# Optimization experiments

Measured on AMD Instinct MI355X. Metric: run time of the kernel, lower is better.

Reference implementation:

```python
import jax, jax.numpy as jnp
import numpy as np

N_NODES = 100000
N_EDGES = 1600000
IN_DIM, HID_DIM, N_CLS = 500, 64, 16


def spline_conv(x, edge_index, edge_attr, w, root, bias):
    """SplineConv with dim=1, kernel_size=2, degree=1, aggr='add'.

    For K=2, m=1 open B-spline: v = pseudo * (K - m) = pseudo in [0,1],
    basis = [(1 - v), v] with kernel indices [0, 1].
    """
    v = jnp.clip(edge_attr[:, 0], 0.0, 1.0 - 1e-6)  # [E]
    src, dst = edge_index[0], edge_index[1]
    # Precompute per-node transforms for both kernel indices (dense GEMMs),
    # then gather per-edge instead of gathering [in,out] weight matrices.
    xw0 = x @ w[0]  # [N, out]
    xw1 = x @ w[1]  # [N, out]
    msg = (1.0 - v)[:, None] * xw0[src] + v[:, None] * xw1[src]  # [E, out]
    agg = jax.ops.segment_sum(msg, dst, num_segments=x.shape[0])  # [N, out]
    return agg + x @ root + bias


def setup_inputs() -> dict:
    key = jax.random.key(0)
    ks = jax.random.split(key, 8)
    x = jax.random.normal(ks[0], (N_NODES, IN_DIM), dtype=jnp.float32)
    edge_index = jax.random.randint(ks[1], (2, N_EDGES), 0, N_NODES, dtype=jnp.int32)
    edge_attr = jax.random.uniform(ks[2], (N_EDGES, 1), dtype=jnp.float32)
    s1 = 1.0 / np.sqrt(IN_DIM)
    s2 = 1.0 / np.sqrt(HID_DIM)
    w1 = jax.random.normal(ks[3], (2, IN_DIM, HID_DIM), dtype=jnp.float32) * s1
    root1 = jax.random.normal(ks[4], (IN_DIM, HID_DIM), dtype=jnp.float32) * s1
    b1 = jnp.zeros((HID_DIM,), dtype=jnp.float32)
    w2 = jax.random.normal(ks[5], (2, HID_DIM, N_CLS), dtype=jnp.float32) * s2
    root2 = jax.random.normal(ks[6], (HID_DIM, N_CLS), dtype=jnp.float32) * s2
    b2 = jnp.zeros((N_CLS,), dtype=jnp.float32)
    return {"x": x, "edge_index": edge_index, "edge_attr": edge_attr,
            "w1": w1, "root1": root1, "b1": b1,
            "w2": w2, "root2": root2, "b2": b2}


def reference(x, edge_index, edge_attr, w1, root1, b1, w2, root2, b2):
    # dropout is identity at inference time
    h = spline_conv(x, edge_index, edge_attr, w1, root1, b1)
    h = jax.nn.relu(h)
    h = spline_conv(h, edge_index, edge_attr, w2, root2, b2)
    return jax.nn.log_softmax(h, axis=1)
```

## Files before the change

### kernel.cpp

```cpp
#include <hip/hip_runtime.h>
#include <math.h>

#define N_NODES 100000
#define N_EDGES 1600000
#define IN_DIM 500
#define HID 64
#define NCLS 16
#define KP 512
#define NSTEPS 16
#define NBUK 391
#define NPAD (NBUK * 256)
#define EPB_B 4096
#define NBB ((N_EDGES + EPB_B - 1) / EPB_B)
#define CAP 8192

typedef __attribute__((ext_vector_type(8))) short short8;
typedef __attribute__((ext_vector_type(4))) float f32x4;

__device__ __forceinline__ unsigned short f2bf(float f) {
    unsigned u = __builtin_bit_cast(unsigned, f);
    return (unsigned short)((u + 0x7FFFu + ((u >> 16) & 1u)) >> 16);
}
__device__ __forceinline__ float bf2f(unsigned short s) {
    unsigned u = ((unsigned)s) << 16;
    return __builtin_bit_cast(float, u);
}
__device__ __forceinline__ unsigned pack2(unsigned short a, unsigned short b) {
    return (unsigned)a | ((unsigned)b << 16);
}
__device__ __forceinline__ void gload16(const void* g, void* l) {
    __builtin_amdgcn_global_load_lds(
        (const __attribute__((address_space(1))) unsigned*)g,
        (__attribute__((address_space(3))) unsigned*)l, 16, 0, 0);
}

__global__ __launch_bounds__(256) void k0_bt(
    const float* __restrict__ w1, const float* __restrict__ root1,
    unsigned short* __restrict__ Bt, int* __restrict__ bkcur)
{
    const int b = blockIdx.x;
    if (b == 192) {
        for (int i = threadIdx.x; i < NBUK; i += 256) bkcur[i] = i * CAP;
        return;
    }
    const float* src;
    int c;
    if (b < 64)        { src = w1;                c = b; }
    else if (b < 128)  { src = w1 + IN_DIM * HID; c = b - 64; }
    else               { src = root1;             c = b - 128; }
    for (int k = threadIdx.x; k < KP; k += 256) {
        float v = (k < IN_DIM) ? src[k * HID + c] : 0.f;
        Bt[b * KP + k] = f2bf(v);
    }
}

union K1Smem {
    struct { float A[4][64 * 32]; unsigned short B[4][192 * 32]; } s;
    unsigned short O[64 * 264];
    struct { int hcnt[NBUK]; int hbase[NBUK]; } bk;
};

__global__ __launch_bounds__(256) void fat_bucket_k1(
    const int* __restrict__ ei, const float* __restrict__ ea,
    int* __restrict__ bkcur, uint2* __restrict__ epk,
    const float* __restrict__ x, const unsigned short* __restrict__ Bt,
    unsigned short* __restrict__ xw01, float* __restrict__ aggH)
{
    __shared__ K1Smem sm;
    const int tid = threadIdx.x;
    const int bi = blockIdx.x;

    if (bi % 5 == 0) {
        const int start = (bi / 5) * EPB_B;
        const int eend = min(start + EPB_B, N_EDGES);

        for (int i = tid; i < NBUK; i += 256) sm.bk.hcnt[i] = 0;
        __syncthreads();

#pragma unroll
        for (int j = 0; j < EPB_B / 256; ++j) {
            const int e = start + j * 256 + tid;
            if (e < eend) atomicAdd(&sm.bk.hcnt[ei[N_EDGES + e] >> 8], 1);
        }
        __syncthreads();

        for (int b = tid; b < NBUK; b += 256) {
            const int c = sm.bk.hcnt[b];
            sm.bk.hbase[b] = c ? atomicAdd(&bkcur[b], c) : 0;
        }
        __syncthreads();
        for (int i = tid; i < NBUK; i += 256) sm.bk.hcnt[i] = 0;
        __syncthreads();

#pragma unroll
        for (int j = 0; j < EPB_B / 256; ++j) {
            const int e = start + j * 256 + tid;
            if (e < eend) {
                const int src = ei[e];
                const int dst = ei[N_EDGES + e];
                const float v = fminf(fmaxf(ea[e], 0.f), 1.f - 1e-6f);
                const unsigned vq = (unsigned)(v * 16777216.0f);
                const int bk = dst >> 8;
                const int r = atomicAdd(&sm.bk.hcnt[bk], 1);
                epk[sm.bk.hbase[bk] + r] =
                    make_uint2((unsigned)src, ((unsigned)(dst & 255) << 24) | vq);
            }
        }
        return;
    }

    const int row0 = (bi - (bi + 4) / 5) * 64;
    const int w = tid >> 6;
    const int l = tid & 63;
    const int l16 = l & 15;
    const int koct = l >> 4;
    const int wr = w >> 1;
    const int wc = w & 1;

    f32x4 acc[2][6];
#pragma unroll
    for (int i = 0; i < 2; ++i)
#pragma unroll
        for (int j = 0; j < 6; ++j) acc[i][j] = (f32x4){0.f, 0.f, 0.f, 0.f};

    const int aChunk4 = (l & 7) * 4;
    const float* aBase[2];
    int aLdsOff[2];
#pragma unroll
    for (int i = 0; i < 2; ++i) {
        const int rowl = (2 * w + i) * 8 + (l >> 3);
        int grow = row0 + rowl;
        if (grow > N_NODES - 1) grow = N_NODES - 1;
        aBase[i] = x + (size_t)grow * IN_DIM;
        aLdsOff[i] = (2 * w + i) * 256;
    }
    const unsigned short* bBase[3];
    int bLdsOff[3];
#pragma unroll
    for (int i = 0; i < 3; ++i) {
        const int coll = (3 * w + i) * 16 + (l >> 2);
        bBase[i] = Bt + (size_t)coll * KP + (l & 3) * 8;
        bLdsOff[i] = (3 * w + i) * 512;
    }

    auto ISSUE = [&](int s) {
        const int k0 = s * 32;
        const int buf = s & 3;
#pragma unroll
        for (int i = 0; i < 2; ++i) {
            int gk = k0 + aChunk4; if (gk > IN_DIM - 4) gk = IN_DIM - 4;
            gload16(aBase[i] + gk, &sm.s.A[buf][aLdsOff[i]]);
        }
#pragma unroll
        for (int i = 0; i < 3; ++i)
            gload16(bBase[i] + k0, &sm.s.B[buf][bLdsOff[i]]);
    };

    ISSUE(0);
    ISSUE(1);
    ISSUE(2);

#pragma unroll
    for (int s = 0; s < NSTEPS; ++s) {
        if (s < NSTEPS - 2)       asm volatile("s_waitcnt vmcnt(10)" ::: "memory");
        else if (s == NSTEPS - 2) asm volatile("s_waitcnt vmcnt(5)" ::: "memory");
        else                      asm volatile("s_waitcnt vmcnt(0)" ::: "memory");
        __builtin_amdgcn_s_barrier();
        asm volatile("" ::: "memory");
        if (s + 3 < NSTEPS) ISSUE(s + 3);

        const int buf = s & 3;
        const float* LA = sm.s.A[buf];
        const unsigned short* LB = sm.s.B[buf];
        short8 af[2];
#pragma unroll
        for (int rb = 0; rb < 2; ++rb) {
            const int r = wr * 32 + rb * 16 + l16;
            f32x4 f0 = *(const f32x4*)&LA[r * 32 + koct * 8];
            f32x4 f1 = *(const f32x4*)&LA[r * 32 + koct * 8 + 4];
            short8 a;
            a[0] = (short)f2bf(f0[0]); a[1] = (short)f2bf(f0[1]);
            a[2] = (short)f2bf(f0[2]); a[3] = (short)f2bf(f0[3]);
            a[4] = (short)f2bf(f1[0]); a[5] = (short)f2bf(f1[1]);
            a[6] = (short)f2bf(f1[2]); a[7] = (short)f2bf(f1[3]);
            af[rb] = a;
        }
#pragma unroll
        for (int cf = 0; cf < 6; ++cf) {
            const int c = wc * 96 + cf * 16 + l16;
            short8 bfg = *(const short8*)&LB[c * 32 + koct * 8];
            acc[0][cf] = __builtin_amdgcn_mfma_f32_16x16x32_bf16(af[0], bfg, acc[0][cf], 0, 0, 0);
            acc[1][cf] = __builtin_amdgcn_mfma_f32_16x16x32_bf16(af[1], bfg, acc[1][cf], 0, 0, 0);
        }
    }
    __syncthreads();

#pragma unroll
    for (int rb = 0; rb < 2; ++rb)
#pragma unroll
        for (int cf = 0; cf < 6; ++cf) {
            const int cg = wc * 96 + cf * 16 + l16;
            if (96 * wc + cf * 16 < 128) {
#pragma unroll
                for (int reg = 0; reg < 4; ++reg) {
                    const int rloc = wr * 32 + rb * 16 + koct * 4 + reg;
                    const int idx = (cg < 64) ? (2 * cg) : (2 * cg - 127);
                    sm.O[rloc * 264 + idx] = f2bf(acc[rb][cf][reg]);
                }
            } else {
#pragma unroll
                for (int reg = 0; reg < 4; ++reg) {
                    const int r = row0 + wr * 32 + rb * 16 + koct * 4 + reg;
                    if (r < N_NODES) aggH[(size_t)r * HID + (cg - 128)] = acc[rb][cf][reg];
                }
            }
        }
    __syncthreads();
    {
        const int row = tid >> 2, q = tid & 3;
        const int rg = row0 + row;
        if (rg < N_NODES) {
#pragma unroll
            for (int j = 0; j < 4; ++j) {
                uint4 v = *(const uint4*)&sm.O[row * 264 + q * 32 + j * 8];
                *(uint4*)&xw01[(size_t)rg * 128 + q * 32 + j * 8] = v;
            }
        }
    }
}

__global__ __launch_bounds__(256) void csr_place(
    const int* __restrict__ bkcur, const uint2* __restrict__ epk,
    uint2* __restrict__ epkS, int* __restrict__ off, int* __restrict__ deg)
{
    __shared__ uint2 buf[CAP];
    __shared__ int hist[256];
    __shared__ int sc[256];
    __shared__ int cur[256];

    const int b = blockIdx.x;
    const int tid = threadIdx.x;
    const int start = b * CAP;
    const int cnt = bkcur[b] - start;

    hist[tid] = 0;
    __syncthreads();
    for (int i = tid; i < cnt; i += 256)
        atomicAdd(&hist[epk[start + i].y >> 24], 1);
    __syncthreads();

    const int val = hist[tid];
    sc[tid] = val;
    for (int d = 1; d < 256; d <<= 1) {
        __syncthreads();
        int add = (tid >= d) ? sc[tid - d] : 0;
        __syncthreads();
        sc[tid] += add;
    }
    __syncthreads();
    const int myloc = sc[tid] - val;
    off[(b << 8) + tid] = start + myloc;
    deg[(b << 8) + tid] = val;
    cur[tid] = myloc;
    __syncthreads();

    for (int i = tid; i < cnt; i += 256) {
        const uint2 u = epk[start + i];
        const int dl = u.y >> 24;
        const float v = (float)(u.y & 0xFFFFFFu) * 5.9604644775390625e-8f;
        const int pos = atomicAdd(&cur[dl], 1);
        buf[pos] = make_uint2(u.x, __builtin_bit_cast(unsigned, v));
    }
    __syncthreads();

    for (int i = tid; i < cnt; i += 256)
        epkS[start + i] = buf[i];
}

__global__ __launch_bounds__(256) void agg1(
    const int* __restrict__ off, const int* __restrict__ deg,
    const uint2* __restrict__ epk, const unsigned* __restrict__ xw01_u,
    float* __restrict__ aggH)
{
    const int n = blockIdx.x * 4 + (threadIdx.x >> 6);
    if (n >= N_NODES) return;
    const int d = threadIdx.x & 63;
    const int start = off[n];
    const int dg = deg[n];

    float acc = aggH[(size_t)n * HID + d];
    for (int i = 0; i < dg; i += 8) {
        unsigned srcs[8];
        float w0[8], w1[8];
#pragma unroll
        for (int j = 0; j < 8; ++j) {
            const bool ok = (i + j) < dg;
            const int idx = ok ? (start + i + j) : start;
            const uint2 t = epk[idx];
            const float v = __builtin_bit_cast(float, t.y);
            srcs[j] = t.x;
            w0[j] = ok ? (1.f - v) : 0.f;
            w1[j] = ok ? v : 0.f;
        }
        unsigned g[8];
#pragma unroll
        for (int j = 0; j < 8; ++j) g[j] = xw01_u[(size_t)srcs[j] * 64 + d];
#pragma unroll
        for (int j = 0; j < 8; ++j) {
            acc += w0[j] * bf2f((unsigned short)(g[j] & 0xFFFF));
            acc += w1[j] * bf2f((unsigned short)(g[j] >> 16));
        }
    }
    aggH[(size_t)n * HID + d] = acc;
}

__global__ __launch_bounds__(256) void k3_relu_gemm(
    const float* __restrict__ aggH, const float* __restrict__ b1,
    const float* __restrict__ w2, const float* __restrict__ root2,
    unsigned* __restrict__ hw01_u, float* __restrict__ agg2)
{
    __shared__ float Ws[3 * HID * NCLS];
    __shared__ float Hs[16][HID];

    const int tid = threadIdx.x;
    for (int i = tid; i < 2 * HID * NCLS; i += 256) Ws[i] = w2[i];
    for (int i = tid; i < HID * NCLS; i += 256) Ws[2 * HID * NCLS + i] = root2[i];

    const int n0 = blockIdx.x * 16;
    for (int i = tid; i < 16 * HID; i += 256) {
        const int nl = i >> 6, k = i & 63;
        const float h = aggH[(size_t)(n0 + nl) * HID + k] + b1[k];
        Hs[nl][k] = fmaxf(h, 0.f);
    }
    __syncthreads();

    const int nl = tid >> 4;
    const int c = tid & 15;
    float a0 = 0.f, a1 = 0.f, a2 = 0.f;
#pragma unroll
    for (int k = 0; k < HID; ++k) {
        const float h = Hs[nl][k];
        a0 += h * Ws[0 * HID * NCLS + k * NCLS + c];
        a1 += h * Ws[1 * HID * NCLS + k * NCLS + c];
        a2 += h * Ws[2 * HID * NCLS + k * NCLS + c];
    }
    const size_t o = (size_t)(n0 + nl) * NCLS + c;
    hw01_u[o] = pack2(f2bf(a0), f2bf(a1));
    agg2[o] = a2;
}

__global__ __launch_bounds__(256) void agg2_sm(
    const int* __restrict__ off, const int* __restrict__ deg,
    const uint2* __restrict__ epk, const unsigned* __restrict__ hw01_u,
    const float* __restrict__ agg2, const float* __restrict__ b2,
    float* __restrict__ out)
{
    const int n = blockIdx.x * 16 + (threadIdx.x >> 4);
    const int c = threadIdx.x & 15;
    const int start = off[n];
    const int dg = deg[n];

    float acc = agg2[(size_t)n * NCLS + c];
    for (int i = 0; i < dg; i += 8) {
        unsigned srcs[8];
        float w0[8], w1[8];
#pragma unroll
        for (int j = 0; j < 8; ++j) {
            const bool ok = (i + j) < dg;
            const int idx = ok ? (start + i + j) : start;
            const uint2 t = epk[idx];
            const float v = __builtin_bit_cast(float, t.y);
            srcs[j] = t.x;
            w0[j] = ok ? (1.f - v) : 0.f;
            w1[j] = ok ? v : 0.f;
        }
        unsigned g[8];
#pragma unroll
        for (int j = 0; j < 8; ++j) g[j] = hw01_u[(size_t)srcs[j] * NCLS + c];
#pragma unroll
        for (int j = 0; j < 8; ++j) {
            acc += w0[j] * bf2f((unsigned short)(g[j] & 0xFFFF));
            acc += w1[j] * bf2f((unsigned short)(g[j] >> 16));
        }
    }

    const float z = acc + b2[c];
    float m = z;
#pragma unroll
    for (int s = 1; s < 16; s <<= 1) m = fmaxf(m, __shfl_xor(m, s, 64));
    const float e = expf(z - m);
    float ssum = e;
#pragma unroll
    for (int s = 1; s < 16; s <<= 1) ssum += __shfl_xor(ssum, s, 64);
    out[(size_t)n * NCLS + c] = (z - m) - logf(ssum);
}

extern "C" void kernel_launch(void* const* d_in, const int* in_sizes, int n_in,
                              void* d_out, int out_size, void* d_ws, size_t ws_size,
                              hipStream_t stream) {
    const float* x = (const float*)d_in[0];
    const int* ei = (const int*)d_in[1];
    const float* ea = (const float*)d_in[2];
    const float* w1 = (const float*)d_in[3];
    const float* root1 = (const float*)d_in[4];
    const float* b1 = (const float*)d_in[5];
    const float* w2 = (const float*)d_in[6];
    const float* root2 = (const float*)d_in[7];
    const float* b2 = (const float*)d_in[8];
    float* out = (float*)d_out;

    char* ws = (char*)d_ws;
    unsigned short* xw01 = (unsigned short*)ws;
    float* aggH = (float*)(ws + 25600000);
    unsigned* hw01_u = (unsigned*)(ws + 51200000);
    float* agg2 = (float*)(ws + 57600000);
    unsigned short* Bt = (unsigned short*)(ws + 64000000);
    int* off = (int*)(ws + 64300000);
    int* deg = (int*)(ws + 64800000);
    int* bkcur = (int*)(ws + 65300000);
    uint2* epk = (uint2*)(ws + 65400000);
    uint2* epkS = (uint2*)(ws + 91100000);

    k0_bt<<<193, 256, 0, stream>>>(w1, root1, Bt, bkcur);

    fat_bucket_k1<<<NBB + (N_NODES + 63) / 64, 256, 0, stream>>>(
        ei, ea, bkcur, epk, x, Bt, xw01, aggH);

    csr_place<<<NBUK, 256, 0, stream>>>(bkcur, epk, epkS, off, deg);
    agg1<<<(N_NODES + 3) / 4, 256, 0, stream>>>(off, deg, epkS, (const unsigned*)xw01, aggH);
    k3_relu_gemm<<<N_NODES / 16, 256, 0, stream>>>(aggH, b1, w2, root2, hw01_u, agg2);
    agg2_sm<<<N_NODES / 16, 256, 0, stream>>>(off, deg, epkS, hw01_u, agg2, b2, out);
}
```

Baseline: 257.4 us.

## Fuse CSR placement with layer-1 aggregation using shared-memory edge buffer

Merges the bucket-sort placement kernel and the first-layer gather aggregation into one 1024-thread kernel per 256-node bucket. After sorting edges into shared memory, each wave aggregates 16 nodes reading edge data straight from LDS rather than re-reading the sorted edge list from global memory. This removes a kernel launch and a global round trip of the edge list. In exchange, only 391 large blocks run the aggregation phase, which can leave parallelism and latency hiding on the gathers lower than the previous 25000-block launch.

```diff
diff --git a/kernel.cpp b/kernel.cpp
--- a/kernel.cpp
+++ b/kernel.cpp
@@ -229,42 +229,50 @@
     }
 }
 
-__global__ __launch_bounds__(256) void csr_place(
+__global__ __launch_bounds__(1024) void place_agg1(
     const int* __restrict__ bkcur, const uint2* __restrict__ epk,
-    uint2* __restrict__ epkS, int* __restrict__ off, int* __restrict__ deg)
+    uint2* __restrict__ epkS, int* __restrict__ off, int* __restrict__ deg,
+    const unsigned* __restrict__ xw01_u, float* __restrict__ aggH)
 {
     __shared__ uint2 buf[CAP];
     __shared__ int hist[256];
     __shared__ int sc[256];
     __shared__ int cur[256];
+    __shared__ int locs[256];
+    __shared__ int degs[256];
 
     const int b = blockIdx.x;
     const int tid = threadIdx.x;
     const int start = b * CAP;
     const int cnt = bkcur[b] - start;
 
-    hist[tid] = 0;
-    __syncthreads();
-    for (int i = tid; i < cnt; i += 256)
+    if (tid < 256) hist[tid] = 0;
+    __syncthreads();
+    for (int i = tid; i < cnt; i += 1024)
         atomicAdd(&hist[epk[start + i].y >> 24], 1);
     __syncthreads();
 
-    const int val = hist[tid];
-    sc[tid] = val;
+    int val = 0;
+    if (tid < 256) { val = hist[tid]; sc[tid] = val; }
+    __syncthreads();
     for (int d = 1; d < 256; d <<= 1) {
-        __syncthreads();
-        int add = (tid >= d) ? sc[tid - d] : 0;
-        __syncthreads();
-        sc[tid] += add;
-    }
-    __syncthreads();
-    const int myloc = sc[tid] - val;
-    off[(b << 8) + tid] = start + myloc;
-    deg[(b << 8) + tid] = val;
-    cur[tid] = myloc;
-    __syncthreads();
-
-    for (int i = tid; i < cnt; i += 256) {
+        int add = 0;
+        if (tid < 256 && tid >= d) add = sc[tid - d];
+        __syncthreads();
+        if (tid < 256) sc[tid] += add;
+        __syncthreads();
+    }
+    if (tid < 256) {
+        const int myloc = sc[tid] - val;
+        off[(b << 8) + tid] = start + myloc;
+        deg[(b << 8) + tid] = val;
+        locs[tid] = myloc;
+        degs[tid] = val;
+        cur[tid] = myloc;
+    }
+    __syncthreads();
+
+    for (int i = tid; i < cnt; i += 1024) {
         const uint2 u = epk[start + i];
         const int dl = u.y >> 24;
         const float v = (float)(u.y & 0xFFFFFFu) * 5.9604644775390625e-8f;
@@ -273,45 +281,44 @@
     }
     __syncthreads();
 
-    for (int i = tid; i < cnt; i += 256)
+    for (int i = tid; i < cnt; i += 1024)
         epkS[start + i] = buf[i];
-}
-
-__global__ __launch_bounds__(256) void agg1(
-    const int* __restrict__ off, const int* __restrict__ deg,
-    const uint2* __restrict__ epk, const unsigned* __restrict__ xw01_u,
-    float* __restrict__ aggH)
-{
-    const int n = blockIdx.x * 4 + (threadIdx.x >> 6);
-    if (n >= N_NODES) return;
-    const int d = threadIdx.x & 63;
-    const int start = off[n];
-    const int dg = deg[n];
-
-    float acc = aggH[(size_t)n * HID + d];
-    for (int i = 0; i < dg; i += 8) {
-        unsigned srcs[8];
-        float w0[8], w1[8];
-#pragma unroll
-        for (int j = 0; j < 8; ++j) {
-            const bool ok = (i + j) < dg;
-            const int idx = ok ? (start + i + j) : start;
-            const uint2 t = epk[idx];
-            const float v = __builtin_bit_cast(float, t.y);
-            srcs[j] = t.x;
-            w0[j] = ok ? (1.f - v) : 0.f;
-            w1[j] = ok ? v : 0.f;
-        }
-        unsigned g[8];
-#pragma unroll
-        for (int j = 0; j < 8; ++j) g[j] = xw01_u[(size_t)srcs[j] * 64 + d];
-#pragma unroll
-        for (int j = 0; j < 8; ++j) {
-            acc += w0[j] * bf2f((unsigned short)(g[j] & 0xFFFF));
-            acc += w1[j] * bf2f((unsigned short)(g[j] >> 16));
-        }
-    }
-    aggH[(size_t)n * HID + d] = acc;
+
+    const int wv = tid >> 6;
+    const int l = tid & 63;
+#pragma unroll
+    for (int t = 0; t < 16; ++t) {
+        const int nl = wv * 16 + t;
+        const int n = (b << 8) + nl;
+        if (n >= N_NODES) continue;
+        const int lst = locs[nl];
+        const int dgn = degs[nl];
+
+        float acc = aggH[(size_t)n * HID + l];
+        for (int i = 0; i < dgn; i += 8) {
+            unsigned srcs[8];
+            float w0[8], w1[8];
+#pragma unroll
+            for (int j = 0; j < 8; ++j) {
+                const bool ok = (i + j) < dgn;
+                const int idx = lst + (ok ? i + j : 0);
+                const uint2 u = buf[idx];
+                const float v = __builtin_bit_cast(float, u.y);
+                srcs[j] = u.x;
+                w0[j] = ok ? (1.f - v) : 0.f;
+                w1[j] = ok ? v : 0.f;
+            }
+            unsigned g[8];
+#pragma unroll
+            for (int j = 0; j < 8; ++j) g[j] = xw01_u[(size_t)srcs[j] * 64 + l];
+#pragma unroll
+            for (int j = 0; j < 8; ++j) {
+                acc += w0[j] * bf2f((unsigned short)(g[j] & 0xFFFF));
+                acc += w1[j] * bf2f((unsigned short)(g[j] >> 16));
+            }
+        }
+        aggH[(size_t)n * HID + l] = acc;
+    }
 }
 
 __global__ __launch_bounds__(256) void k3_relu_gemm(
@@ -426,8 +433,8 @@
     fat_bucket_k1<<<NBB + (N_NODES + 63) / 64, 256, 0, stream>>>(
         ei, ea, bkcur, epk, x, Bt, xw01, aggH);
 
-    csr_place<<<NBUK, 256, 0, stream>>>(bkcur, epk, epkS, off, deg);
-    agg1<<<(N_NODES + 3) / 4, 256, 0, stream>>>(off, deg, epkS, (const unsigned*)xw01, aggH);
+    place_agg1<<<NBUK, 1024, 0, stream>>>(bkcur, epk, epkS, off, deg,
+                                          (const unsigned*)xw01, aggH);
     k3_relu_gemm<<<N_NODES / 16, 256, 0, stream>>>(aggH, b1, w2, root2, hw01_u, agg2);
     agg2_sm<<<N_NODES / 16, 256, 0, stream>>>(off, deg, epkS, hw01_u, agg2, b2, out);
 }
```

Result: faster. 244.0 us (-5.2%).
